# Kernel tuning notes

Measured on AMD Instinct MI355X. Metric: run time of the kernel, lower is better.

Reference implementation:

```python
import jax, jax.numpy as jnp
import numpy as np

V, E, H, L, B = 32000, 128, 32, 64, 32


def setup_inputs() -> dict:
    key = jax.random.key(0)
    k0, k1, k2, k3, k4, k5 = jax.random.split(key, 6)
    stdv = 1.0 / np.sqrt(H)
    we = jax.random.uniform(k0, (V, E), minval=-stdv, maxval=stdv, dtype=jnp.float32)
    we = we.at[1].set(0.0)  # pad token row zeroed, as in original
    i2h1 = jax.random.uniform(k1, (E + H, H), minval=-stdv, maxval=stdv, dtype=jnp.float32)
    i2h2 = jax.random.uniform(k2, (E + H, H), minval=-stdv, maxval=stdv, dtype=jnp.float32)
    h2o = jax.random.uniform(k3, (2 * H, V), minval=-stdv, maxval=stdv, dtype=jnp.float32)
    bias = jnp.ones((1, H), dtype=jnp.float32)  # assigned after reset_parameters -> stays ones
    hidden_init = jax.random.normal(k4, (1, H), dtype=jnp.float32)  # plain buffer, not reset
    inp = jax.random.randint(k5, (L, B), 0, V, dtype=jnp.int64)
    return {"inp": inp, "we": we, "i2h1": i2h1, "i2h2": i2h2,
            "h2o": h2o, "bias": bias, "hidden_init": hidden_init}


def reference(inp, we, i2h1, i2h2, h2o, bias, hidden_init):
    Lr, Br = inp.shape
    Hh = hidden_init.shape[1]
    emb = we[inp]                                   # [L,B,E] embedding gather
    h0 = jnp.broadcast_to(hidden_init, (Br, Hh))    # [B,H]
    b = jnp.broadcast_to(bias, (Br, Hh))            # [B,H]

    def make_step(W):
        def step(h, e):
            h_new = jnp.tanh(jnp.concatenate([e, h], axis=1) @ W + b)
            return h_new, h_new
        return step

    # forward direction: hf[i] = hidden after consuming token i
    _, hf = jax.lax.scan(make_step(i2h1), h0, emb)
    # backward direction (scan over reversed time, flip back)
    _, hb_rev = jax.lax.scan(make_step(i2h2), h0, emb[::-1])
    hb = hb_rev[::-1]                               # hb[i] = bwd hidden after token i

    # original uses hiddenf[i] (pre-token-i fwd state) and hiddenb[i+1] (post-token-(i+1) bwd state)
    hf_used = jnp.concatenate([h0[None], hf[:-1]], axis=0)   # [L,B,H]
    hb_used = jnp.concatenate([hb[1:], h0[None]], axis=0)    # [L,B,H]

    hcat = jnp.concatenate([hf_used, hb_used], axis=-1)      # [L,B,2H]
    logits = jnp.einsum('lbh,hv->lbv', hcat, h2o)            # [L,B,V]
    return jax.nn.log_softmax(logits, axis=-1)
```

## Files before the change

### kernel.cpp

```cpp
#include <hip/hip_runtime.h>
#include <hip/hip_cooperative_groups.h>

namespace cg = cooperative_groups;

#define V_SZ 32000
#define E_SZ 128
#define H_SZ 32
#define L_SZ 64
#define B_SZ 32
#define M_TOT 2048
#define K2 64
#define NVT 125
#define GRID_F 1000

typedef __bf16 bf16x8 __attribute__((ext_vector_type(8)));
typedef float f32x4 __attribute__((ext_vector_type(4)));

__device__ __forceinline__ unsigned short f2bf(float f) {
    unsigned int u = __float_as_uint(f);
    u += 0x7FFFu + ((u >> 16) & 1u);
    return (unsigned short)(u >> 16);
}

__device__ __forceinline__ void load_vfrag(
    const __bf16* __restrict__ h2oT, int vbase, int lg, int lr,
    bf16x8 vf[4][2]) {
#pragma unroll
    for (int i = 0; i < 4; ++i) {
        const __bf16* vp = h2oT + (size_t)(vbase + i * 16 + lr) * K2 + lg * 8;
        vf[i][0] = *(const bf16x8*)(vp);
        vf[i][1] = *(const bf16x8*)(vp + 32);
    }
}

__device__ __forceinline__ void load_hfrag(
    const __bf16* __restrict__ hcat, int rowbase, int lg, int lr,
    bf16x8 hf[4][2]) {
#pragma unroll
    for (int j = 0; j < 4; ++j) {
        const __bf16* hp = hcat + (size_t)(rowbase + j * 16 + lr) * K2 + lg * 8;
        hf[j][0] = *(const bf16x8*)(hp);
        hf[j][1] = *(const bf16x8*)(hp + 32);
    }
}

__device__ __forceinline__ void tile_gemm_t(
    const bf16x8 vf[4][2], const bf16x8 hf[4][2], f32x4 acc[4][4]) {
#pragma unroll
    for (int i = 0; i < 4; ++i)
#pragma unroll
        for (int j = 0; j < 4; ++j) acc[i][j] = (f32x4){0.f, 0.f, 0.f, 0.f};
#pragma unroll
    for (int i = 0; i < 4; ++i)
#pragma unroll
        for (int j = 0; j < 4; ++j) {
            acc[i][j] = __builtin_amdgcn_mfma_f32_16x16x32_bf16(vf[i][0], hf[j][0], acc[i][j], 0, 0, 0);
            acc[i][j] = __builtin_amdgcn_mfma_f32_16x16x32_bf16(vf[i][1], hf[j][1], acc[i][j], 0, 0, 0);
        }
}

template <typename EP>
__device__ __forceinline__ void sweep4(
    const __bf16* __restrict__ hcat, int y0, int lg, int lr, EP&& ep) {
    bf16x8 hfA[4][2], hfB[4][2];
    load_hfrag(hcat, y0, lg, lr, hfA);
    load_hfrag(hcat, y0 + 64, lg, lr, hfB);
    ep(hfA, y0);
    load_hfrag(hcat, y0 + 128, lg, lr, hfA);
    ep(hfB, y0 + 64);
    load_hfrag(hcat, y0 + 192, lg, lr, hfB);
    ep(hfA, y0 + 128);
    ep(hfB, y0 + 192);
}

struct EpA {
    const bf16x8 (*vf)[2];
    float* S;
    int lane;
    __device__ __forceinline__ void operator()(const bf16x8 hf[4][2], int rowbase) const {
        f32x4 acc[4][4];
        tile_gemm_t((const bf16x8(*)[2])vf, hf, acc);
        float srow[4];
#pragma unroll
        for (int j = 0; j < 4; ++j) {
            float s = 0.f;
#pragma unroll
            for (int i = 0; i < 4; ++i)
#pragma unroll
                for (int r = 0; r < 4; ++r) s += __expf(acc[i][j][r]);
            srow[j] = s;
        }
#pragma unroll
        for (int j = 0; j < 4; ++j) {
            srow[j] += __shfl_xor(srow[j], 16, 64);
            srow[j] += __shfl_xor(srow[j], 32, 64);
        }
        if (lane < 16) {
#pragma unroll
            for (int j = 0; j < 4; ++j)
                atomicAdd(&S[rowbase + j * 16 + lane], srow[j]);
        }
    }
};

struct EpB {
    const bf16x8 (*vf)[2];
    const float* S;
    float* out;
    int vbase, lg, lr;
    __device__ __forceinline__ void operator()(const bf16x8 hf[4][2], int rowbase) const {
        float lsev[4];
#pragma unroll
        for (int j = 0; j < 4; ++j)
            lsev[j] = logf(S[rowbase + j * 16 + lr]);
        f32x4 acc[4][4];
        tile_gemm_t((const bf16x8(*)[2])vf, hf, acc);
#pragma unroll
        for (int j = 0; j < 4; ++j) {
            float* rp = out + (size_t)(rowbase + j * 16 + lr) * V_SZ + vbase + lg * 4;
#pragma unroll
            for (int i = 0; i < 4; ++i) {
                f32x4 v;
                v.x = acc[i][j].x - lsev[j];
                v.y = acc[i][j].y - lsev[j];
                v.z = acc[i][j].z - lsev[j];
                v.w = acc[i][j].w - lsev[j];
                *(f32x4*)(rp + i * 16) = v;
            }
        }
    }
};

__device__ __forceinline__ void transpose_unit(
    int p, int tid, const float* __restrict__ h2o,
    unsigned short* __restrict__ h2oT_u) {
    const int v = p * 64 + (tid & 63);
    const int kg = tid >> 6;
    unsigned int* dst = (unsigned int*)(h2oT_u + (size_t)v * K2 + kg * 16);
#pragma unroll
    for (int kk = 0; kk < 16; kk += 2) {
        const int k = kg * 16 + kk;
        float a = h2o[(size_t)k * V_SZ + v];
        float b = h2o[(size_t)(k + 1) * V_SZ + v];
        dst[kk >> 1] = (unsigned int)f2bf(a) | ((unsigned int)f2bf(b) << 16);
    }
}

__device__ __forceinline__ void rnn_unit(
    int w2, int tid, float* Xl, const int* __restrict__ inp,
    const float* __restrict__ we, const float* __restrict__ i2h1,
    const float* __restrict__ i2h2, const float* __restrict__ bias,
    const float* __restrict__ hinit, unsigned short* __restrict__ hcat_u) {
    const int dir = w2 >> 4;
    const int bpair = w2 & 15;
    const float* W = dir ? i2h2 : i2h1;
    {
        const int j = tid & 31, bb = (tid >> 5) & 1, to = tid >> 6;
        const int b = bpair * 2 + bb;
        const float bj = bias[j];
        for (int tt = 0; tt < 16; ++tt) {
            const int t = to * 16 + tt;
            const int idx = inp[t * B_SZ + b];
            const float* er = we + (size_t)idx * E_SZ;
            float acc = bj;
#pragma unroll
            for (int k0 = 0; k0 < E_SZ; k0 += 4) {
                f32x4 e4 = *(const f32x4*)(er + k0);
                acc += e4.x * W[(k0 + 0) * H_SZ + j];
                acc += e4.y * W[(k0 + 1) * H_SZ + j];
                acc += e4.z * W[(k0 + 2) * H_SZ + j];
                acc += e4.w * W[(k0 + 3) * H_SZ + j];
            }
            Xl[(t * 2 + bb) * H_SZ + j] = acc;
        }
    }
    __syncthreads();
    if (tid < 64) {
        const int lane = tid;
        const int bb = lane >> 5;
        const int b = bpair * 2 + bb;
        const int j = lane & 31;
        const int srcbase = lane & 32;
        float wh[H_SZ];
#pragma unroll
        for (int k = 0; k < H_SZ; ++k) wh[k] = W[(E_SZ + k) * H_SZ + j];
        float h = hinit[j];
        for (int step = 0; step < L_SZ; ++step) {
            const int tt = dir ? (L_SZ - 1 - step) : step;
            hcat_u[(tt * B_SZ + b) * K2 + dir * H_SZ + j] = f2bf(h);
            float a0 = Xl[(tt * 2 + bb) * H_SZ + j];
            float a1 = 0.f, a2 = 0.f, a3 = 0.f;
#pragma unroll
            for (int k = 0; k < H_SZ; k += 4) {
                a0 += __shfl(h, srcbase | k, 64) * wh[k];
                a1 += __shfl(h, srcbase | (k + 1), 64) * wh[k + 1];
                a2 += __shfl(h, srcbase | (k + 2), 64) * wh[k + 2];
                a3 += __shfl(h, srcbase | (k + 3), 64) * wh[k + 3];
            }
            float x2 = (a0 + a1) + (a2 + a3);
            float e = __expf(2.f * x2);
            h = 1.f - 2.f * __builtin_amdgcn_rcpf(e + 1.f);
        }
    }
}

__global__ __launch_bounds__(256, 4) void k_fused(
    const int* __restrict__ inp, const float* __restrict__ we,
    const float* __restrict__ i2h1, const float* __restrict__ i2h2,
    const float* __restrict__ h2o, const float* __restrict__ bias,
    const float* __restrict__ hinit,
    unsigned short* __restrict__ hcat_u, unsigned short* __restrict__ h2oT_u,
    float* __restrict__ S, float* __restrict__ out) {
    cg::grid_group gg = cg::this_grid();
    __shared__ float Xl[L_SZ * 2 * H_SZ];
    const int tid = threadIdx.x;
    const int p = blockIdx.x;
    const int wave = tid >> 6, lane = tid & 63;
    const int lg = lane >> 4, lr = lane & 15;

    if (p < 500) {
        transpose_unit(p, tid, h2o, h2oT_u);
    } else if (p < 532) {
        rnn_unit(p - 500, tid, Xl, inp, we, i2h1, i2h2, bias, hinit, hcat_u);
    } else if (p == 532) {
        for (int i = tid; i < M_TOT; i += 256) S[i] = 0.f;
    }
    __threadfence();
    gg.sync();

    const __bf16* hcat = (const __bf16*)hcat_u;
    const __bf16* h2oT = (const __bf16*)h2oT_u;
    const int xcol = p >> 3;
    const int y0 = (p & 7) * 256;
    const int vbase = xcol * 256 + wave * 64;

    bf16x8 vf[4][2];
    load_vfrag(h2oT, vbase, lg, lr, vf);

    EpA epa{vf, S, lane};
    sweep4(hcat, y0, lg, lr, epa);
    __threadfence();
    gg.sync();

    EpB epb{vf, S, out, vbase, lg, lr};
    sweep4(hcat, y0, lg, lr, epb);
}

__global__ __launch_bounds__(256) void k_prep_rnn(
    const int* __restrict__ inp, const float* __restrict__ we,
    const float* __restrict__ i2h1, const float* __restrict__ i2h2,
    const float* __restrict__ h2o, const float* __restrict__ bias,
    const float* __restrict__ hinit,
    unsigned short* __restrict__ hcat_u, unsigned short* __restrict__ h2oT_u,
    float* __restrict__ S) {
    __shared__ float Xl[L_SZ * 2 * H_SZ];
    const int tid = threadIdx.x;
    const int p = blockIdx.x;
    if (p < 500) {
        if (p == 0)
            for (int i = tid; i < M_TOT; i += 256) S[i] = 0.f;
        transpose_unit(p, tid, h2o, h2oT_u);
        return;
    }
    rnn_unit(p - 500, tid, Xl, inp, we, i2h1, i2h2, bias, hinit, hcat_u);
}

__global__ __launch_bounds__(256) void k_pass_a(
    const __bf16* __restrict__ hcat, const __bf16* __restrict__ h2oT,
    float* __restrict__ S) {
    const int tid = threadIdx.x;
    const int wave = tid >> 6, lane = tid & 63;
    const int lg = lane >> 4, lr = lane & 15;
    const int y0 = blockIdx.y * 256;
    const int vbase = blockIdx.x * 256 + wave * 64;
    bf16x8 vf[4][2];
    load_vfrag(h2oT, vbase, lg, lr, vf);
    EpA epa{vf, S, lane};
    sweep4(hcat, y0, lg, lr, epa);
}

__global__ __launch_bounds__(256) void k_pass_b(
    const __bf16* __restrict__ hcat, const __bf16* __restrict__ h2oT,
    const float* __restrict__ S, float* __restrict__ out) {
    const int tid = threadIdx.x;
    const int wave = tid >> 6, lane = tid & 63;
    const int lg = lane >> 4, lr = lane & 15;
    const int y0 = blockIdx.y * 256;
    const int vbase = blockIdx.x * 256 + wave * 64;
    bf16x8 vf[4][2];
    load_vfrag(h2oT, vbase, lg, lr, vf);
    EpB epb{vf, S, out, vbase, lg, lr};
    sweep4(hcat, y0, lg, lr, epb);
}

extern "C" void kernel_launch(void* const* d_in, const int* in_sizes, int n_in,
                              void* d_out, int out_size, void* d_ws, size_t ws_size,
                              hipStream_t stream) {
    (void)in_sizes; (void)n_in; (void)out_size; (void)ws_size;
    const int*   inp   = (const int*)d_in[0];
    const float* we    = (const float*)d_in[1];
    const float* i2h1  = (const float*)d_in[2];
    const float* i2h2  = (const float*)d_in[3];
    const float* h2o   = (const float*)d_in[4];
    const float* bias  = (const float*)d_in[5];
    const float* hinit = (const float*)d_in[6];
    float* out = (float*)d_out;
    char* ws = (char*)d_ws;
    unsigned short* hcat_u = (unsigned short*)(ws);
    unsigned short* h2oT_u = (unsigned short*)(ws + 262144);
    float*          S      = (float*)(ws + 4358144);

    hipError_t e = hipErrorUnknown;
    int occ = 0;
    if (hipOccupancyMaxActiveBlocksPerMultiprocessor(&occ, k_fused, 256, 0)
            == hipSuccess && occ * 256 >= GRID_F) {
        void* args[] = {
            (void*)&inp, (void*)&we, (void*)&i2h1, (void*)&i2h2, (void*)&h2o,
            (void*)&bias, (void*)&hinit, (void*)&hcat_u, (void*)&h2oT_u,
            (void*)&S, (void*)&out};
        e = hipLaunchCooperativeKernel((void*)k_fused, dim3(GRID_F), dim3(256),
                                       args, 0, stream);
    }
    if (e != hipSuccess) {
        k_prep_rnn<<<532, 256, 0, stream>>>(inp, we, i2h1, i2h2, h2o, bias,
                                            hinit, hcat_u, h2oT_u, S);
        k_pass_a<<<dim3(NVT, 8), 256, 0, stream>>>(
            (const __bf16*)hcat_u, (const __bf16*)h2oT_u, S);
        k_pass_b<<<dim3(NVT, 8), 256, 0, stream>>>(
            (const __bf16*)hcat_u, (const __bf16*)h2oT_u, S, out);
    }
}
```

Measured before the change: 158.5 us.

## Split prep/RNN phase out of cooperative kernel into separate launch

```diff
diff --git a/kernel.cpp b/kernel.cpp
--- a/kernel.cpp
+++ b/kernel.cpp
@@ -131,29 +131,37 @@
     }
 };
 
-__device__ __forceinline__ void transpose_unit(
-    int p, int tid, const float* __restrict__ h2o,
-    unsigned short* __restrict__ h2oT_u) {
-    const int v = p * 64 + (tid & 63);
-    const int kg = tid >> 6;
-    unsigned int* dst = (unsigned int*)(h2oT_u + (size_t)v * K2 + kg * 16);
-#pragma unroll
-    for (int kk = 0; kk < 16; kk += 2) {
-        const int k = kg * 16 + kk;
-        float a = h2o[(size_t)k * V_SZ + v];
-        float b = h2o[(size_t)(k + 1) * V_SZ + v];
-        dst[kk >> 1] = (unsigned int)f2bf(a) | ((unsigned int)f2bf(b) << 16);
-    }
-}
-
-__device__ __forceinline__ void rnn_unit(
-    int w2, int tid, float* Xl, const int* __restrict__ inp,
-    const float* __restrict__ we, const float* __restrict__ i2h1,
-    const float* __restrict__ i2h2, const float* __restrict__ bias,
-    const float* __restrict__ hinit, unsigned short* __restrict__ hcat_u) {
+__global__ __launch_bounds__(256) void k_prep_rnn(
+    const int* __restrict__ inp, const float* __restrict__ we,
+    const float* __restrict__ i2h1, const float* __restrict__ i2h2,
+    const float* __restrict__ h2o, const float* __restrict__ bias,
+    const float* __restrict__ hinit,
+    unsigned short* __restrict__ hcat_u, unsigned short* __restrict__ h2oT_u,
+    float* __restrict__ S) {
+    const int tid = threadIdx.x;
+    const int p = blockIdx.x;
+    if (p < 500) {
+        if (p == 0) {
+#pragma unroll
+            for (int i = tid; i < M_TOT; i += 256) S[i] = 0.f;
+        }
+        const int v = p * 64 + (tid & 63);
+        const int kg = tid >> 6;
+        unsigned int* dst = (unsigned int*)(h2oT_u + (size_t)v * K2 + kg * 16);
+#pragma unroll
+        for (int kk = 0; kk < 16; kk += 2) {
+            const int k = kg * 16 + kk;
+            float a = h2o[(size_t)k * V_SZ + v];
+            float b = h2o[(size_t)(k + 1) * V_SZ + v];
+            dst[kk >> 1] = (unsigned int)f2bf(a) | ((unsigned int)f2bf(b) << 16);
+        }
+        return;
+    }
+    const int w2 = p - 500;
     const int dir = w2 >> 4;
     const int bpair = w2 & 15;
     const float* W = dir ? i2h2 : i2h1;
+    __shared__ float Xl[L_SZ * 2 * H_SZ];
     {
         const int j = tid & 31, bb = (tid >> 5) & 1, to = tid >> 6;
         const int b = bpair * 2 + bb;
@@ -204,65 +212,31 @@
     }
 }
 
-__global__ __launch_bounds__(256, 4) void k_fused(
-    const int* __restrict__ inp, const float* __restrict__ we,
-    const float* __restrict__ i2h1, const float* __restrict__ i2h2,
-    const float* __restrict__ h2o, const float* __restrict__ bias,
-    const float* __restrict__ hinit,
-    unsigned short* __restrict__ hcat_u, unsigned short* __restrict__ h2oT_u,
+__global__ __launch_bounds__(256) void k_fused(
+    const unsigned short* __restrict__ hcat_u,
+    const unsigned short* __restrict__ h2oT_u,
     float* __restrict__ S, float* __restrict__ out) {
     cg::grid_group gg = cg::this_grid();
-    __shared__ float Xl[L_SZ * 2 * H_SZ];
     const int tid = threadIdx.x;
-    const int p = blockIdx.x;
     const int wave = tid >> 6, lane = tid & 63;
     const int lg = lane >> 4, lr = lane & 15;
-
-    if (p < 500) {
-        transpose_unit(p, tid, h2o, h2oT_u);
-    } else if (p < 532) {
-        rnn_unit(p - 500, tid, Xl, inp, we, i2h1, i2h2, bias, hinit, hcat_u);
-    } else if (p == 532) {
-        for (int i = tid; i < M_TOT; i += 256) S[i] = 0.f;
-    }
+    const int xcol = blockIdx.x >> 3;
+    const int y0 = (blockIdx.x & 7) * 256;
+    const int vbase = xcol * 256 + wave * 64;
+    const __bf16* hcat = (const __bf16*)hcat_u;
+    const __bf16* h2oT = (const __bf16*)h2oT_u;
+
+    bf16x8 vf[4][2];
+    load_vfrag(h2oT, vbase, lg, lr, vf);
+
+    EpA epa{vf, S, lane};
+    sweep4(hcat, y0, lg, lr, epa);
+
     __threadfence();
     gg.sync();
 
-    const __bf16* hcat = (const __bf16*)hcat_u;
-    const __bf16* h2oT = (const __bf16*)h2oT_u;
-    const int xcol = p >> 3;
-    const int y0 = (p & 7) * 256;
-    const int vbase = xcol * 256 + wave * 64;
-
-    bf16x8 vf[4][2];
-    load_vfrag(h2oT, vbase, lg, lr, vf);
-
-    EpA epa{vf, S, lane};
-    sweep4(hcat, y0, lg, lr, epa);
-    __threadfence();
-    gg.sync();
-
     EpB epb{vf, S, out, vbase, lg, lr};
     sweep4(hcat, y0, lg, lr, epb);
-}
-
-__global__ __launch_bounds__(256) void k_prep_rnn(
-    const int* __restrict__ inp, const float* __restrict__ we,
-    const float* __restrict__ i2h1, const float* __restrict__ i2h2,
-    const float* __restrict__ h2o, const float* __restrict__ bias,
-    const float* __restrict__ hinit,
-    unsigned short* __restrict__ hcat_u, unsigned short* __restrict__ h2oT_u,
-    float* __restrict__ S) {
-    __shared__ float Xl[L_SZ * 2 * H_SZ];
-    const int tid = threadIdx.x;
-    const int p = blockIdx.x;
-    if (p < 500) {
-        if (p == 0)
-            for (int i = tid; i < M_TOT; i += 256) S[i] = 0.f;
-        transpose_unit(p, tid, h2o, h2oT_u);
-        return;
-    }
-    rnn_unit(p - 500, tid, Xl, inp, we, i2h1, i2h2, bias, hinit, hcat_u);
 }
 
 __global__ __launch_bounds__(256) void k_pass_a(
@@ -310,20 +284,18 @@
     unsigned short* h2oT_u = (unsigned short*)(ws + 262144);
     float*          S      = (float*)(ws + 4358144);
 
+    k_prep_rnn<<<532, 256, 0, stream>>>(inp, we, i2h1, i2h2, h2o, bias, hinit,
+                                        hcat_u, h2oT_u, S);
+
     hipError_t e = hipErrorUnknown;
     int occ = 0;
     if (hipOccupancyMaxActiveBlocksPerMultiprocessor(&occ, k_fused, 256, 0)
             == hipSuccess && occ * 256 >= GRID_F) {
-        void* args[] = {
-            (void*)&inp, (void*)&we, (void*)&i2h1, (void*)&i2h2, (void*)&h2o,
-            (void*)&bias, (void*)&hinit, (void*)&hcat_u, (void*)&h2oT_u,
-            (void*)&S, (void*)&out};
+        void* args[] = {(void*)&hcat_u, (void*)&h2oT_u, (void*)&S, (void*)&out};
         e = hipLaunchCooperativeKernel((void*)k_fused, dim3(GRID_F), dim3(256),
                                        args, 0, stream);
     }
     if (e != hipSuccess) {
-        k_prep_rnn<<<532, 256, 0, stream>>>(inp, we, i2h1, i2h2, h2o, bias,
-                                            hinit, hcat_u, h2oT_u, S);
         k_pass_a<<<dim3(NVT, 8), 256, 0, stream>>>(
             (const __bf16*)hcat_u, (const __bf16*)h2oT_u, S);
         k_pass_b<<<dim3(NVT, 8), 256, 0, stream>>>(
```

Result: no change. 158.5 us (-0.0%).
